# Kernel tuning notes

Hardware: AMD Instinct MI355X
Metric: run time of the kernel (lower is better)

Reference implementation:

```python
import jax, jax.numpy as jnp
import numpy as np

# ---- geometry constants (from init_kwargs) ----
ANGLE_NUM = 360
DET = 448          # detector bins
N = 320            # volume is N x N, voxel pitch 1.0, centered at origin
SID = 500.0        # source-isocenter distance
SDD = 1000.0       # source-detector distance
DU = 1.6           # detector pixel pitch
LAMB = 1.0
R = N * np.sqrt(2.0) / 2.0   # half-diagonal of volume
N_SAMP = 452                 # samples per ray, step ~ 1 voxel
DT = np.float32(2.0 * R / N_SAMP)


def forward_project(vol):
    """Ray-driven fan-beam forward projection. vol: [B,N,N] -> sino [B,A,D]."""
    half = (N - 1) / 2.0
    betas = jnp.deg2rad(jnp.linspace(0.0, 360.0, ANGLE_NUM, endpoint=False)).astype(jnp.float32)
    u = ((jnp.arange(DET, dtype=jnp.float32) - (DET - 1) / 2.0) * DU)          # [D]
    t = (SID - R) + (jnp.arange(N_SAMP, dtype=jnp.float32) + 0.5) * (2.0 * R / N_SAMP)  # [S]

    def one_angle(_, beta):
        cb, sb = jnp.cos(beta), jnp.sin(beta)
        src = jnp.stack([SID * cb, SID * sb])            # source position [2]
        ax = jnp.stack([-cb, -sb])                       # toward isocenter
        uax = jnp.stack([-sb, cb])                       # detector axis
        det_pts = src[None, :] + SDD * ax[None, :] + u[:, None] * uax[None, :]  # [D,2]
        dirs = det_pts - src[None, :]
        dirs = dirs / jnp.linalg.norm(dirs, axis=-1, keepdims=True)             # [D,2]
        pts = src[None, None, :] + t[None, :, None] * dirs[:, None, :]          # [D,S,2]
        ix = pts[..., 0] + half
        iy = pts[..., 1] + half
        x0 = jnp.floor(ix); y0 = jnp.floor(iy)
        fx = ix - x0;       fy = iy - y0
        x0i = x0.astype(jnp.int32); y0i = y0.astype(jnp.int32)

        def gather(yy, xx):
            inb = (xx >= 0) & (xx < N) & (yy >= 0) & (yy < N)
            v = vol[:, jnp.clip(yy, 0, N - 1), jnp.clip(xx, 0, N - 1)]  # [B,D,S]
            return v * inb[None].astype(vol.dtype)

        val = (gather(y0i, x0i)         * ((1 - fx) * (1 - fy))[None]
             + gather(y0i, x0i + 1)     * (fx * (1 - fy))[None]
             + gather(y0i + 1, x0i)     * ((1 - fx) * fy)[None]
             + gather(y0i + 1, x0i + 1) * (fx * fy)[None])
        return None, val.sum(-1) * DT   # line integral per detector bin [B,D]

    _, sino = jax.lax.scan(one_angle, None, betas)   # [A,B,D]
    return jnp.transpose(sino, (1, 0, 2))            # [B,A,D]


def setup_inputs() -> dict:
    key = jax.random.key(0)
    k1, k2 = jax.random.split(key)
    x = jax.random.normal(k1, (2, N, N), dtype=jnp.float32)
    p = jax.random.normal(k2, (2, ANGLE_NUM, DET), dtype=jnp.float32)
    return {"x": x, "p": p}


def reference(x, p):
    # SART-style update: x - lamb * BP(FP(x) - p), BP = exact adjoint of FP
    residual = forward_project(x) - p
    (bp_vol,) = jax.linear_transpose(forward_project, x)(residual)
    return x - LAMB * bp_vol
```

## Files before the change

### kernel.cpp

```cpp
#include <hip/hip_runtime.h>
#include <hip/hip_fp16.h>
#include <math.h>

#define A_NUM 360
#define DET_N 448
#define NN 320
#define NSAMP 452
#define NB 2
#define NPIX (NN * NN)
#define NRAY (A_NUM * DET_N)
#define NCH 4
#define CHS (NSAMP / NCH)
#define NORB 25600
#define NSPQ15 15
#define NSPQ12 12
#define PN 324

#define R_D   226.27416997969522
#define DT_D  (2.0 * R_D / (double)NSAMP)
#define T0_D  (500.0 - R_D + 0.5 * DT_D)
#define DTF   ((float)DT_D)
#define T0F   ((float)T0_D)
#define INVDT ((float)(1.0 / DT_D))
#define K0F   ((float)((-1.4150 - T0_D) * (1.0 / DT_D)))

typedef float f32x2 __attribute__((ext_vector_type(2)));

__device__ __forceinline__ int orb_swizzle(int ri, int rj) {
    int tile = (rj >> 3) * 20 + (ri >> 3);
    int intra = ((rj & 7) << 3) | (ri & 7);
    return (tile << 6) | intra;
}

__global__ __launch_bounds__(256) void prep_k(float2* __restrict__ tabD,
                                              float4* __restrict__ tabS,
                                              float4* __restrict__ dirq,
                                              float4* __restrict__ angG) {
    int tid = blockIdx.x * blockDim.x + threadIdx.x;
    if (tid >= NRAY) return;
    int d = tid % DET_N, a = tid / DET_N;
    double beta = (double)a * (M_PI / 180.0);
    double cbd = cos(beta), sbd = sin(beta);
    double u = ((double)d - 223.5) * 1.6;
    double inorm = 1.0 / sqrt(1.0e6 + u * u);
    float dx = (float)((-1000.0 * cbd - u * sbd) * inorm);
    float dy = (float)((-1000.0 * sbd + u * cbd) * inorm);
    tabD[tid] = make_float2(dx, dy);
    if (d == 0) {
        tabS[a] = make_float4((float)cbd, (float)sbd,
                              (float)(500.0 * cbd + 161.5),
                              (float)(500.0 * sbd + 161.5));
        angG[a] = make_float4((float)cbd, (float)sbd,
                              (float)(500.0 * cbd + 159.5),
                              (float)(500.0 * sbd + 159.5));
    }
    if (a < 90) dirq[a * DET_N + d] = make_float4(dx, dy, DTF * dx, DTF * dy);
}

__device__ __forceinline__ unsigned packpix(const float* __restrict__ x,
                                            bool v, int idx) {
    if (!v) return 0u;
    __half2 h = __floats2half2_rn(x[idx], x[NPIX + idx]);
    return *reinterpret_cast<unsigned*>(&h);
}
__device__ __forceinline__ f32x2 up16(unsigned w) {
    __half2 h = *reinterpret_cast<__half2*>(&w);
    return (f32x2){__low2float(h), __high2float(h)};
}

__global__ __launch_bounds__(256) void interleaveQB_k(const float* __restrict__ x,
                                                      uint4* __restrict__ xb) {
    int t = blockIdx.x * blockDim.x + threadIdx.x;
    if (t >= PN * PN) return;
    int px = t % PN, py = t / PN;
    int ox = px - 2, oy = py - 2;
    bool cx0 = (ox >= 0) && (ox < NN);
    bool cx1 = (ox + 1 >= 0) && (ox + 1 < NN);
    bool cy0 = (oy >= 0) && (oy < NN);
    bool cy1 = (oy + 1 >= 0) && (oy + 1 < NN);
    int b = oy * NN + ox;
    uint4 w;
    w.x = packpix(x, cx0 && cy0, b);
    w.y = packpix(x, cx1 && cy0, b + 1);
    w.z = packpix(x, cx0 && cy1, b + NN);
    w.w = packpix(x, cx1 && cy1, b + NN + 1);
    xb[t] = w;
}

__global__ __launch_bounds__(256) void interleaveQBT_k(const float* __restrict__ x,
                                                       uint4* __restrict__ xbT) {
    int t = blockIdx.x * blockDim.x + threadIdx.x;
    if (t >= PN * PN) return;
    int r = t % PN, q = t / PN;
    int row0 = r - 2, col0 = q - 2;
    bool r0v = (row0 >= 0) && (row0 < NN);
    bool r1v = (row0 + 1 >= 0) && (row0 + 1 < NN);
    bool c0v = (col0 >= 0) && (col0 < NN);
    bool c1v = (col0 + 1 >= 0) && (col0 + 1 < NN);
    int b = row0 * NN + col0;
    uint4 w;
    w.x = packpix(x, r0v && c0v, b);
    w.y = packpix(x, r1v && c0v, b + NN);
    w.z = packpix(x, r0v && c1v, b + 1);
    w.w = packpix(x, r1v && c1v, b + NN + 1);
    xbT[t] = w;
}

__device__ __forceinline__ void samp1(const uint4* __restrict__ buf,
                                      float ix, float iy,
                                      f32x2& accA, f32x2& accB) {
    float xf = floorf(ix), yf = floorf(iy);
    float fx = ix - xf, fy = iy - yf;
    int idx = (int)yf * PN + (int)xf;
    uint4 qv = buf[idx];
    float gx = 1.0f - fx, gy = 1.0f - fy;
    float w00 = gx * gy, w01 = fx * gy, w10 = gx * fy, w11 = fx * fy;
    accA = __builtin_elementwise_fma((f32x2){w00, w00}, up16(qv.x), accA);
    accB = __builtin_elementwise_fma((f32x2){w01, w01}, up16(qv.y), accB);
    accA = __builtin_elementwise_fma((f32x2){w10, w10}, up16(qv.z), accA);
    accB = __builtin_elementwise_fma((f32x2){w11, w11}, up16(qv.w), accB);
}

__global__ __launch_bounds__(256) void partial_k(const float2* __restrict__ tabD,
                                                 const float4* __restrict__ tabS,
                                                 const uint4* __restrict__ bufR,
                                                 const uint4* __restrict__ bufT,
                                                 float2* __restrict__ part) {
    int tid = blockIdx.x * blockDim.x + threadIdx.x;
    if (tid >= NRAY * NCH) return;
    int d_lo = tid & 15;
    int c    = (tid >> 4) & 3;
    int rest = tid >> 6;
    int d_hi = rest % (DET_N / 16);
    int a    = rest / (DET_N / 16);
    int ray  = a * DET_N + d_hi * 16 + d_lo;

    float2 D = tabD[ray];
    float4 S = tabS[a];
    bool swp = fabsf(S.x) > fabsf(S.y);
    float dirx = swp ? D.y : D.x;
    float diry = swp ? D.x : D.y;
    float sx   = swp ? S.w : S.z;
    float sy   = swp ? S.z : S.w;
    const uint4* __restrict__ buf = swp ? bufT : bufR;

    float invx = __builtin_amdgcn_rcpf(dirx);
    float invy = __builtin_amdgcn_rcpf(diry);
    float tx1 = (0.5f   - sx) * invx;
    float tx2 = (322.5f - sx) * invx;
    float ty1 = (0.5f   - sy) * invy;
    float ty2 = (322.5f - sy) * invy;
    float tmn = fmaxf(fminf(tx1, tx2), fminf(ty1, ty2));
    float tmx = fminf(fmaxf(tx1, tx2), fmaxf(ty1, ty2));
    float smnf = fminf(fmaxf(ceilf((tmn - T0F) * INVDT), 0.0f), (float)(NSAMP - 1));
    float smxf = fminf(fmaxf(floorf((tmx - T0F) * INVDT), 0.0f), (float)(NSAMP - 1));
    int smin = (int)smnf;
    int smax = (int)smxf;
    int klo = (smin - c + 3) >> 2;  if (klo < 0) klo = 0;
    int khi = (smax - c) >> 2;      if (khi > CHS - 1) khi = CHS - 1;
    int kn = khi - klo + 1;

    float t0c = fmaf((float)(c + 4 * klo), DTF, T0F);
    float ix = fmaf(t0c, dirx, sx);
    float iy = fmaf(t0c, diry, sy);
    float stx = (4.0f * DTF) * dirx;
    float sty = (4.0f * DTF) * diry;

    f32x2 accA = {0.0f, 0.0f}, accB = {0.0f, 0.0f};

    int k = 0;
#pragma unroll 2
    for (; k + 4 <= kn; k += 4) {
        float ix0 = ix,              iy0 = iy;
        float ix1 = ix + stx,        iy1 = iy + sty;
        float ix2 = ix + 2.0f * stx, iy2 = iy + 2.0f * sty;
        float ix3 = ix + 3.0f * stx, iy3 = iy + 3.0f * sty;
        float xf0 = floorf(ix0), yf0 = floorf(iy0);
        float xf1 = floorf(ix1), yf1 = floorf(iy1);
        float xf2 = floorf(ix2), yf2 = floorf(iy2);
        float xf3 = floorf(ix3), yf3 = floorf(iy3);
        int i0 = (int)yf0 * PN + (int)xf0;
        int i1 = (int)yf1 * PN + (int)xf1;
        int i2 = (int)yf2 * PN + (int)xf2;
        int i3 = (int)yf3 * PN + (int)xf3;
        uint4 q0 = buf[i0];
        uint4 q1 = buf[i1];
        uint4 q2 = buf[i2];
        uint4 q3 = buf[i3];
        float fx0 = ix0 - xf0, fy0 = iy0 - yf0;
        float fx1 = ix1 - xf1, fy1 = iy1 - yf1;
        float fx2 = ix2 - xf2, fy2 = iy2 - yf2;
        float fx3 = ix3 - xf3, fy3 = iy3 - yf3;
        float gx0 = 1.0f - fx0, gy0 = 1.0f - fy0;
        float gx1 = 1.0f - fx1, gy1 = 1.0f - fy1;
        float gx2 = 1.0f - fx2, gy2 = 1.0f - fy2;
        float gx3 = 1.0f - fx3, gy3 = 1.0f - fy3;
        float w;
        w = gx0 * gy0; accA = __builtin_elementwise_fma((f32x2){w, w}, up16(q0.x), accA);
        w = fx0 * gy0; accB = __builtin_elementwise_fma((f32x2){w, w}, up16(q0.y), accB);
        w = gx0 * fy0; accA = __builtin_elementwise_fma((f32x2){w, w}, up16(q0.z), accA);
        w = fx0 * fy0; accB = __builtin_elementwise_fma((f32x2){w, w}, up16(q0.w), accB);
        w = gx1 * gy1; accA = __builtin_elementwise_fma((f32x2){w, w}, up16(q1.x), accA);
        w = fx1 * gy1; accB = __builtin_elementwise_fma((f32x2){w, w}, up16(q1.y), accB);
        w = gx1 * fy1; accA = __builtin_elementwise_fma((f32x2){w, w}, up16(q1.z), accA);
        w = fx1 * fy1; accB = __builtin_elementwise_fma((f32x2){w, w}, up16(q1.w), accB);
        w = gx2 * gy2; accA = __builtin_elementwise_fma((f32x2){w, w}, up16(q2.x), accA);
        w = fx2 * gy2; accB = __builtin_elementwise_fma((f32x2){w, w}, up16(q2.y), accB);
        w = gx2 * fy2; accA = __builtin_elementwise_fma((f32x2){w, w}, up16(q2.z), accA);
        w = fx2 * fy2; accB = __builtin_elementwise_fma((f32x2){w, w}, up16(q2.w), accB);
        w = gx3 * gy3; accA = __builtin_elementwise_fma((f32x2){w, w}, up16(q3.x), accA);
        w = fx3 * gy3; accB = __builtin_elementwise_fma((f32x2){w, w}, up16(q3.y), accB);
        w = gx3 * fy3; accA = __builtin_elementwise_fma((f32x2){w, w}, up16(q3.z), accA);
        w = fx3 * fy3; accB = __builtin_elementwise_fma((f32x2){w, w}, up16(q3.w), accB);
        ix += 4.0f * stx; iy += 4.0f * sty;
    }
    for (; k < kn; ++k) {
        samp1(buf, ix, iy, accA, accB);
        ix += stx; iy += sty;
    }

    f32x2 acc = accA + accB;
    part[c * NRAY + ray] = make_float2(acc.x, acc.y);
}

__global__ __launch_bounds__(256) void finalize4_k(const float* __restrict__ p,
                                                   const float2* __restrict__ part,
                                                   float4* __restrict__ rvq) {
    int tid = blockIdx.x * blockDim.x + threadIdx.x;
    if (tid >= 90 * DET_N) return;
    int d = tid % DET_N, am = tid / DET_N;
    float rv[8];
#pragma unroll
    for (int k = 0; k < 4; ++k) {
        int ray = (am + 90 * k) * DET_N + d;
        float a0 = 0.0f, a1 = 0.0f;
#pragma unroll
        for (int c = 0; c < NCH; ++c) {
            float2 pr = part[c * NRAY + ray];
            a0 += pr.x; a1 += pr.y;
        }
        rv[2 * k]     = -fmaf(a0, DTF, -p[ray]) * DTF;
        rv[2 * k + 1] = -fmaf(a1, DTF, -p[NRAY + ray]) * DTF;
    }
    rvq[2 * tid]     = make_float4(rv[0], rv[1], rv[2], rv[3]);
    rvq[2 * tid + 1] = make_float4(rv[4], rv[5], rv[6], rv[7]);
}

#define TAP4(A0, A1, A2, A3)                                 \
    {                                                        \
        f32x2 ad  = __builtin_elementwise_max(dxy, -dxy);    \
        f32x2 wv2 = __builtin_elementwise_max(one2 - ad, zero2); \
        float w = wv2.x * wv2.y;                             \
        f32x2 wv = {w, w};                                   \
        A0 = __builtin_elementwise_fma(wv, q0, A0);          \
        A1 = __builtin_elementwise_fma(wv, q1, A1);          \
        A2 = __builtin_elementwise_fma(wv, q2, A2);          \
        A3 = __builtin_elementwise_fma(wv, q3, A3);          \
        dxy += dd2;                                          \
    }

#define QTAPS(Q, A0, A1, A2, A3, DX_, DY_, EX_, EY_)                       \
    {                                                                      \
        float4 A = angG[90 * (Q) + am];                                    \
        float rx = fi - A.z, ry = fj - A.w;                                \
        float rpar  = -fmaf(rx, A.x, ry * A.y);                            \
        float rperp = fmaf(ry, A.x, -rx * A.y);                            \
        float us = 1000.0f * rperp * __builtin_amdgcn_rcpf(rpar);          \
        float dstar = fmaf(us, 0.625f, 223.5f);                            \
        float r2 = fmaf(rx, rx, ry * ry);                                  \
        float ir = rsqrtf(r2);                                             \
        float g  = fmaf(fabsf(rx) + fabsf(ry), ir, 0.031f);                \
        float kk = fmaf(us, us, 1.0e6f) * ir;                              \
        float dd = fmaf(g * kk, 6.25e-4f, 0.05f);                          \
        int dlo = (int)ceilf(dstar - dd);  if (dlo < 0) dlo = 0;           \
        int dhi = (int)floorf(dstar + dd); if (dhi > DET_N - 1) dhi = DET_N - 1; \
        for (int d = dlo; d <= dhi; ++d) {                                 \
            float4 Dq  = sD[d];                                            \
            float4 r01 = sR0[d];                                           \
            float4 r23 = sR1[d];                                           \
            float Tx = DX_, Ty = DY_;                                      \
            float ts = fmaf(rx, Tx, ry * Ty);                              \
            float sf = ceilf(fmaf(ts, INVDT, K0F));                        \
            sf = fminf(fmaxf(sf, 0.0f), (float)(NSAMP - 3));               \
            float tt = fmaf(sf, DTF, T0F);                                 \
            f32x2 dxy = {fmaf(tt, Tx, -rx), fmaf(tt, Ty, -ry)};            \
            f32x2 dd2 = {EX_, EY_};                                        \
            f32x2 q0 = {r01.x, r01.y}, q1 = {r01.z, r01.w};                \
            f32x2 q2 = {r23.x, r23.y}, q3 = {r23.z, r23.w};                \
            TAP4(A0, A1, A2, A3)                                           \
            TAP4(A0, A1, A2, A3)                                           \
            TAP4(A0, A1, A2, A3)                                           \
        }                                                                  \
    }

template <int NSPLIT>
__global__ __launch_bounds__(256) void bp4_k(const float4* __restrict__ dirq,
                                             const float4* __restrict__ rvq,
                                             const float4* __restrict__ angG,
                                             float* __restrict__ bpp) {
    __shared__ float4 sD[DET_N];
    __shared__ float4 sR0[DET_N];
    __shared__ float4 sR1[DET_N];

    int tid = blockIdx.x * blockDim.x + threadIdx.x;
    int orb = tid % NORB;
    int sp  = tid / NORB;
    int tile  = orb >> 6;
    int intra = orb & 63;
    int ri = (tile % 20) * 8 + (intra & 7);
    int rj = (tile / 20) * 8 + (intra >> 3);
    float fi = (float)ri, fj = (float)rj;

    const f32x2 one2 = {1.0f, 1.0f}, zero2 = {0.0f, 0.0f};
    f32x2 acc0 = {0.0f, 0.0f}, acc1 = acc0, acc2 = acc0, acc3 = acc0;

    bool first = true;
    for (int am = sp; am < 90; am += NSPLIT) {
        const float4* Drow = dirq + am * DET_N;
        const float4* Rrow = rvq + am * DET_N * 2;
        if (!first) __syncthreads();
        first = false;
        for (int i = threadIdx.x; i < DET_N; i += 256) {
            sD[i]  = Drow[i];
            sR0[i] = Rrow[2 * i];
            sR1[i] = Rrow[2 * i + 1];
        }
        __syncthreads();

        QTAPS(0, acc0, acc1, acc2, acc3,  Dq.x,  Dq.y,  Dq.z,  Dq.w)
        QTAPS(1, acc3, acc0, acc1, acc2, -Dq.y,  Dq.x, -Dq.w,  Dq.z)
        QTAPS(2, acc2, acc3, acc0, acc1, -Dq.x, -Dq.y, -Dq.z, -Dq.w)
        QTAPS(3, acc1, acc2, acc3, acc0,  Dq.y, -Dq.x,  Dq.w, -Dq.z)
    }

    int base = sp * 8 * NORB + orb;
    bpp[base           ] = acc0.x;
    bpp[base + 1 * NORB] = acc0.y;
    bpp[base + 2 * NORB] = acc1.x;
    bpp[base + 3 * NORB] = acc1.y;
    bpp[base + 4 * NORB] = acc2.x;
    bpp[base + 5 * NORB] = acc2.y;
    bpp[base + 6 * NORB] = acc3.x;
    bpp[base + 7 * NORB] = acc3.y;
}

template <int NSPLIT>
__global__ __launch_bounds__(256) void combine4_k(const float* __restrict__ x,
                                                  const float* __restrict__ bpp,
                                                  float* __restrict__ out) {
    int tid = blockIdx.x * blockDim.x + threadIdx.x;
    if (tid >= NB * NPIX) return;
    int i = tid % NN;
    int j = (tid / NN) % NN;
    int b = tid / NPIX;
    int k, ri, rj;
    if (j < 160) {
        if (i < 160) { k = 0; ri = i;       rj = j;       }
        else         { k = 1; ri = j;       rj = 319 - i; }
    } else {
        if (i >= 160){ k = 2; ri = 319 - i; rj = 319 - j; }
        else         { k = 3; ri = 319 - j; rj = i;       }
    }
    int off = (k * 2 + b) * NORB + orb_swizzle(ri, rj);
    float s = x[tid];
#pragma unroll
    for (int sp = 0; sp < NSPLIT; ++sp) s += bpp[sp * 8 * NORB + off];
    out[tid] = s;
}

template <bool USE_TAB>
__global__ __launch_bounds__(256) void residual_k(const float* __restrict__ x,
                                                  const float* __restrict__ p,
                                                  void* __restrict__ tabv) {
    int tid = blockIdx.x * blockDim.x + threadIdx.x;
    if (tid >= NRAY) return;
    int d = tid % DET_N, a = tid / DET_N;
    double beta = (double)a * (M_PI / 180.0);
    double cbd = cos(beta), sbd = sin(beta);
    double u = ((double)d - 223.5) * 1.6;
    double inorm = 1.0 / sqrt(1.0e6 + u * u);
    float dirx = (float)((-1000.0 * cbd - u * sbd) * inorm);
    float diry = (float)((-1000.0 * sbd + u * cbd) * inorm);
    float sx = (float)(500.0 * cbd + 159.5);
    float sy = (float)(500.0 * sbd + 159.5);
    const float* __restrict__ v0 = x;
    const float* __restrict__ v1 = x + NPIX;
    float acc0 = 0.0f, acc1 = 0.0f;
    for (int s = 0; s < NSAMP; ++s) {
        float t  = fmaf((float)s, DTF, T0F);
        float ix = fmaf(t, dirx, sx);
        float iy = fmaf(t, diry, sy);
        float xf = floorf(ix), yf = floorf(iy);
        int x0 = (int)xf, y0 = (int)yf;
        if (x0 < -1 || x0 >= NN || y0 < -1 || y0 >= NN) continue;
        float fx = ix - xf, fy = iy - yf;
        int x1 = x0 + 1, y1 = y0 + 1;
        bool vx0 = (x0 >= 0), vx1 = (x1 < NN);
        bool vy0 = (y0 >= 0), vy1 = (y1 < NN);
        int x0c = vx0 ? x0 : 0, x1c = vx1 ? x1 : NN - 1;
        int y0c = vy0 ? y0 : 0, y1c = vy1 ? y1 : NN - 1;
        int i00 = y0c * NN + x0c, i01 = y0c * NN + x1c;
        int i10 = y1c * NN + x0c, i11 = y1c * NN + x1c;
        float gx = 1.0f - fx, gy = 1.0f - fy;
        float w00 = (vx0 && vy0) ? gx * gy : 0.0f;
        float w01 = (vx1 && vy0) ? fx * gy : 0.0f;
        float w10 = (vx0 && vy1) ? gx * fy : 0.0f;
        float w11 = (vx1 && vy1) ? fx * fy : 0.0f;
        acc0 = fmaf(v0[i00], w00, acc0); acc0 = fmaf(v0[i01], w01, acc0);
        acc0 = fmaf(v0[i10], w10, acc0); acc0 = fmaf(v0[i11], w11, acc0);
        acc1 = fmaf(v1[i00], w00, acc1); acc1 = fmaf(v1[i01], w01, acc1);
        acc1 = fmaf(v1[i10], w10, acc1); acc1 = fmaf(v1[i11], w11, acc1);
    }
    float rv0 = -fmaf(acc0, DTF, -p[tid]) * DTF;
    float rv1 = -fmaf(acc1, DTF, -p[NRAY + tid]) * DTF;
    if constexpr (USE_TAB) {
        ((float4*)tabv)[tid] = make_float4(dirx, diry, rv0, rv1);
    } else {
        ((float2*)tabv)[tid] = make_float2(rv0, rv1);
    }
}

template <int NSPLIT, bool DIRECT, bool USE_TAB>
__global__ __launch_bounds__(256) void bp_k(const void* __restrict__ tabv,
                                            const float* __restrict__ x,
                                            float* __restrict__ outp) {
    __shared__ float4 ang[A_NUM];
    for (int a = threadIdx.x; a < A_NUM; a += blockDim.x) {
        double beta = (double)a * (M_PI / 180.0);
        double cbd = cos(beta), sbd = sin(beta);
        ang[a] = make_float4((float)cbd, (float)sbd,
                             (float)(500.0 * cbd + 159.5),
                             (float)(500.0 * sbd + 159.5));
    }
    __syncthreads();

    int tid = blockIdx.x * blockDim.x + threadIdx.x;
    if (tid >= NPIX * NSPLIT) return;
    int pix = tid % NPIX;
    int sp  = tid / NPIX;
    float fi = (float)(pix % NN), fj = (float)(pix / NN);

    float acc0 = 0.0f, acc1 = 0.0f;

    for (int a = sp; a < A_NUM; a += NSPLIT) {
        float4 A = ang[a];
        float rx = fi - A.z, ry = fj - A.w;
        float rpar  = -fmaf(rx, A.x, ry * A.y);
        float rperp = fmaf(ry, A.x, -rx * A.y);
        float us = 1000.0f * rperp * __builtin_amdgcn_rcpf(rpar);
        float dstar = fmaf(us, 0.625f, 223.5f);
        float r2 = fmaf(rx, rx, ry * ry);
        float kk = fmaf(us, us, 1.0e6f) * rsqrtf(r2);
        float dd = fmaf(kk, 8.8394e-4f, 0.05f);
        int dlo = (int)ceilf(dstar - dd);  if (dlo < 0) dlo = 0;
        int dhi = (int)floorf(dstar + dd); if (dhi > DET_N - 1) dhi = DET_N - 1;

        const float4* __restrict__ Trow =
            USE_TAB ? ((const float4*)tabv) + a * DET_N : nullptr;
        const float2* __restrict__ RVrow =
            USE_TAB ? nullptr : ((const float2*)tabv) + a * DET_N;

        for (int d = dlo; d <= dhi; ++d) {
            float dirx, diry, rv0, rv1;
            if constexpr (USE_TAB) {
                float4 T = Trow[d];
                dirx = T.x; diry = T.y; rv0 = T.z; rv1 = T.w;
            } else {
                float u = ((float)d - 223.5f) * 1.6f;
                float inv = rsqrtf(fmaf(u, u, 1.0e6f));
                dirx = fmaf(-1000.0f, A.x, -u * A.y) * inv;
                diry = fmaf(-1000.0f, A.y,  u * A.x) * inv;
                float2 RV = RVrow[d];
                rv0 = RV.x; rv1 = RV.y;
            }
            float ts = fmaf(rx, dirx, ry * diry);
            float sf = ceilf(fmaf(ts, INVDT, K0F));
            sf = fminf(fmaxf(sf, 0.0f), (float)(NSAMP - 3));
            float tt = fmaf(sf, DTF, T0F);
            float dx = fmaf(tt, dirx, -rx);
            float dy = fmaf(tt, diry, -ry);
            float ddx = DTF * dirx, ddy = DTF * diry;
#pragma unroll
            for (int k = 0; k < 3; ++k) {
                float wx = fmaxf(1.0f - fabsf(dx), 0.0f);
                float wy = fmaxf(1.0f - fabsf(dy), 0.0f);
                float w = wx * wy;
                acc0 = fmaf(w, rv0, acc0);
                acc1 = fmaf(w, rv1, acc1);
                dx += ddx; dy += ddy;
            }
        }
    }

    if constexpr (DIRECT) {
        outp[pix]        = x[pix]        + acc0;
        outp[NPIX + pix] = x[NPIX + pix] + acc1;
    } else {
        outp[(sp * 2 + 0) * NPIX + pix] = acc0;
        outp[(sp * 2 + 1) * NPIX + pix] = acc1;
    }
}

template <int NSPLIT>
__global__ __launch_bounds__(256) void combine_k(const float* __restrict__ x,
                                                 const float* __restrict__ part,
                                                 float* __restrict__ out) {
    int tid = blockIdx.x * blockDim.x + threadIdx.x;
    if (tid >= NB * NPIX) return;
    int pix = tid % NPIX, b = tid / NPIX;
    float s = x[tid];
#pragma unroll
    for (int sp = 0; sp < NSPLIT; ++sp) s += part[(sp * 2 + b) * NPIX + pix];
    out[tid] = s;
}

extern "C" void kernel_launch(void* const* d_in, const int* in_sizes, int n_in,
                              void* d_out, int out_size, void* d_ws, size_t ws_size,
                              hipStream_t stream) {
    const float* x = (const float*)d_in[0];
    const float* p = (const float*)d_in[1];
    float* out = (float*)d_out;
    char* ws = (char*)d_ws;

    const size_t bpp15_bytes = (size_t)NSPQ15 * 8 * NORB * 4;
    const size_t bpp12_bytes = (size_t)NSPQ12 * 8 * NORB * 4;
    const size_t NEED15 = 1951744 + bpp15_bytes;
    const size_t NEED12 = 1951744 + bpp12_bytes;
    const size_t NEED8  = 10471936;

    const size_t tab_bytes  = sizeof(float4) * NRAY;
    const size_t bpp4_bytes = sizeof(float) * 8 * NPIX;

    if (ws_size >= NEED12 || ws_size >= NEED8) {
        float4* dirq  = (float4*)(ws + 0);
        float2* tabD  = (float2*)(ws + 645120);
        float4* rvq   = (float4*)(ws + 645120);
        float4* tabS  = (float4*)(ws + 1935360);
        float4* angG  = (float4*)(ws + 1943552);
        uint4*  xqb   = (uint4*)(ws + 1951744);
        uint4*  xqbT  = (uint4*)(ws + 3631360);
        float2* fpart = (float2*)(ws + 5310976);
        float*  bpp   = (float*)(ws + 1951744);

        prep_k<<<NRAY / 256, 256, 0, stream>>>(tabD, tabS, dirq, angG);
        interleaveQB_k<<<(PN * PN + 255) / 256, 256, 0, stream>>>(x, xqb);
        interleaveQBT_k<<<(PN * PN + 255) / 256, 256, 0, stream>>>(x, xqbT);
        partial_k<<<(NRAY * NCH) / 256, 256, 0, stream>>>(tabD, tabS, xqb, xqbT, fpart);
        finalize4_k<<<(90 * DET_N + 255) / 256, 256, 0, stream>>>(p, fpart, rvq);
        if (ws_size >= NEED15) {
            bp4_k<NSPQ15><<<(NORB * NSPQ15) / 256, 256, 0, stream>>>(dirq, rvq, angG, bpp);
            combine4_k<NSPQ15><<<(NB * NPIX) / 256, 256, 0, stream>>>(x, bpp, out);
        } else if (ws_size >= NEED12) {
            bp4_k<NSPQ12><<<(NORB * NSPQ12) / 256, 256, 0, stream>>>(dirq, rvq, angG, bpp);
            combine4_k<NSPQ12><<<(NB * NPIX) / 256, 256, 0, stream>>>(x, bpp, out);
        } else {
            bp4_k<8><<<(NORB * 8) / 256, 256, 0, stream>>>(dirq, rvq, angG, bpp);
            combine4_k<8><<<(NB * NPIX) / 256, 256, 0, stream>>>(x, bpp, out);
        }
    } else if (ws_size >= tab_bytes + bpp4_bytes) {
        float4* tab = (float4*)ws;
        float* bpp  = (float*)(ws + tab_bytes);
        residual_k<true><<<(NRAY + 255) / 256, 256, 0, stream>>>(x, p, tab);
        bp_k<4, false, true><<<(NPIX * 4) / 256, 256, 0, stream>>>(tab, x, bpp);
        combine_k<4><<<(NB * NPIX + 255) / 256, 256, 0, stream>>>(x, bpp, out);
    } else if (ws_size >= tab_bytes) {
        float4* tab = (float4*)ws;
        residual_k<true><<<(NRAY + 255) / 256, 256, 0, stream>>>(x, p, tab);
        bp_k<1, true, true><<<NPIX / 256, 256, 0, stream>>>(tab, x, out);
    } else {
        float2* rw2 = (float2*)ws;
        residual_k<false><<<(NRAY + 255) / 256, 256, 0, stream>>>(x, p, rw2);
        bp_k<1, true, false><<<NPIX / 256, 256, 0, stream>>>(rw2, x, out);
    }
}
```

Baseline: 143.4 us.

## Software-pipeline forward-projection gathers and shrink backprojection direction table

```diff
diff --git a/kernel.cpp b/kernel.cpp
--- a/kernel.cpp
+++ b/kernel.cpp
@@ -34,7 +34,7 @@
 
 __global__ __launch_bounds__(256) void prep_k(float2* __restrict__ tabD,
                                               float4* __restrict__ tabS,
-                                              float4* __restrict__ dirq,
+                                              float2* __restrict__ dirq,
                                               float4* __restrict__ angG) {
     int tid = blockIdx.x * blockDim.x + threadIdx.x;
     if (tid >= NRAY) return;
@@ -54,7 +54,7 @@
                               (float)(500.0 * cbd + 159.5),
                               (float)(500.0 * sbd + 159.5));
     }
-    if (a < 90) dirq[a * DET_N + d] = make_float4(dx, dy, DTF * dx, DTF * dy);
+    if (a < 90) dirq[a * DET_N + d] = make_float2(dx, dy);
 }
 
 __device__ __forceinline__ unsigned packpix(const float* __restrict__ x,
@@ -121,6 +121,52 @@
     accB = __builtin_elementwise_fma((f32x2){w11, w11}, up16(qv.w), accB);
 }
 
+#define PLOAD(Q0, Q1, Q2, Q3, FX, FY)                                  \
+    {                                                                  \
+        float x0_ = lx,               y0_ = ly;                        \
+        float x1_ = lx + stx,         y1_ = ly + sty;                  \
+        float x2_ = lx + 2.0f * stx,  y2_ = ly + 2.0f * sty;           \
+        float x3_ = lx + 3.0f * stx,  y3_ = ly + 3.0f * sty;           \
+        float xf0_ = floorf(x0_), yf0_ = floorf(y0_);                  \
+        float xf1_ = floorf(x1_), yf1_ = floorf(y1_);                  \
+        float xf2_ = floorf(x2_), yf2_ = floorf(y2_);                  \
+        float xf3_ = floorf(x3_), yf3_ = floorf(y3_);                  \
+        Q0 = buf[(int)yf0_ * PN + (int)xf0_];                          \
+        Q1 = buf[(int)yf1_ * PN + (int)xf1_];                          \
+        Q2 = buf[(int)yf2_ * PN + (int)xf2_];                          \
+        Q3 = buf[(int)yf3_ * PN + (int)xf3_];                          \
+        FX##0 = x0_ - xf0_; FY##0 = y0_ - yf0_;                        \
+        FX##1 = x1_ - xf1_; FY##1 = y1_ - yf1_;                        \
+        FX##2 = x2_ - xf2_; FY##2 = y2_ - yf2_;                        \
+        FX##3 = x3_ - xf3_; FY##3 = y3_ - yf3_;                        \
+        lx += 4.0f * stx; ly += 4.0f * sty;                            \
+    }
+
+#define PCONS(Q0, Q1, Q2, Q3, FX, FY)                                  \
+    {                                                                  \
+        float gx0_ = 1.0f - FX##0, gy0_ = 1.0f - FY##0;                \
+        float gx1_ = 1.0f - FX##1, gy1_ = 1.0f - FY##1;                \
+        float gx2_ = 1.0f - FX##2, gy2_ = 1.0f - FY##2;                \
+        float gx3_ = 1.0f - FX##3, gy3_ = 1.0f - FY##3;                \
+        float w_;                                                      \
+        w_ = gx0_ * gy0_;  accA = __builtin_elementwise_fma((f32x2){w_, w_}, up16(Q0.x), accA); \
+        w_ = FX##0 * gy0_; accB = __builtin_elementwise_fma((f32x2){w_, w_}, up16(Q0.y), accB); \
+        w_ = gx0_ * FY##0; accA = __builtin_elementwise_fma((f32x2){w_, w_}, up16(Q0.z), accA); \
+        w_ = FX##0 * FY##0;accB = __builtin_elementwise_fma((f32x2){w_, w_}, up16(Q0.w), accB); \
+        w_ = gx1_ * gy1_;  accA = __builtin_elementwise_fma((f32x2){w_, w_}, up16(Q1.x), accA); \
+        w_ = FX##1 * gy1_; accB = __builtin_elementwise_fma((f32x2){w_, w_}, up16(Q1.y), accB); \
+        w_ = gx1_ * FY##1; accA = __builtin_elementwise_fma((f32x2){w_, w_}, up16(Q1.z), accA); \
+        w_ = FX##1 * FY##1;accB = __builtin_elementwise_fma((f32x2){w_, w_}, up16(Q1.w), accB); \
+        w_ = gx2_ * gy2_;  accA = __builtin_elementwise_fma((f32x2){w_, w_}, up16(Q2.x), accA); \
+        w_ = FX##2 * gy2_; accB = __builtin_elementwise_fma((f32x2){w_, w_}, up16(Q2.y), accB); \
+        w_ = gx2_ * FY##2; accA = __builtin_elementwise_fma((f32x2){w_, w_}, up16(Q2.z), accA); \
+        w_ = FX##2 * FY##2;accB = __builtin_elementwise_fma((f32x2){w_, w_}, up16(Q2.w), accB); \
+        w_ = gx3_ * gy3_;  accA = __builtin_elementwise_fma((f32x2){w_, w_}, up16(Q3.x), accA); \
+        w_ = FX##3 * gy3_; accB = __builtin_elementwise_fma((f32x2){w_, w_}, up16(Q3.y), accB); \
+        w_ = gx3_ * FY##3; accA = __builtin_elementwise_fma((f32x2){w_, w_}, up16(Q3.z), accA); \
+        w_ = FX##3 * FY##3;accB = __builtin_elementwise_fma((f32x2){w_, w_}, up16(Q3.w), accB); \
+    }
+
 __global__ __launch_bounds__(256) void partial_k(const float2* __restrict__ tabD,
                                                  const float4* __restrict__ tabS,
                                                  const uint4* __restrict__ bufR,
@@ -159,64 +205,43 @@
     int klo = (smin - c + 3) >> 2;  if (klo < 0) klo = 0;
     int khi = (smax - c) >> 2;      if (khi > CHS - 1) khi = CHS - 1;
     int kn = khi - klo + 1;
+    if (kn < 0) kn = 0;
 
     float t0c = fmaf((float)(c + 4 * klo), DTF, T0F);
-    float ix = fmaf(t0c, dirx, sx);
-    float iy = fmaf(t0c, diry, sy);
+    float lx = fmaf(t0c, dirx, sx);
+    float ly = fmaf(t0c, diry, sy);
     float stx = (4.0f * DTF) * dirx;
     float sty = (4.0f * DTF) * diry;
 
     f32x2 accA = {0.0f, 0.0f}, accB = {0.0f, 0.0f};
 
-    int k = 0;
-#pragma unroll 2
-    for (; k + 4 <= kn; k += 4) {
-        float ix0 = ix,              iy0 = iy;
-        float ix1 = ix + stx,        iy1 = iy + sty;
-        float ix2 = ix + 2.0f * stx, iy2 = iy + 2.0f * sty;
-        float ix3 = ix + 3.0f * stx, iy3 = iy + 3.0f * sty;
-        float xf0 = floorf(ix0), yf0 = floorf(iy0);
-        float xf1 = floorf(ix1), yf1 = floorf(iy1);
-        float xf2 = floorf(ix2), yf2 = floorf(iy2);
-        float xf3 = floorf(ix3), yf3 = floorf(iy3);
-        int i0 = (int)yf0 * PN + (int)xf0;
-        int i1 = (int)yf1 * PN + (int)xf1;
-        int i2 = (int)yf2 * PN + (int)xf2;
-        int i3 = (int)yf3 * PN + (int)xf3;
-        uint4 q0 = buf[i0];
-        uint4 q1 = buf[i1];
-        uint4 q2 = buf[i2];
-        uint4 q3 = buf[i3];
-        float fx0 = ix0 - xf0, fy0 = iy0 - yf0;
-        float fx1 = ix1 - xf1, fy1 = iy1 - yf1;
-        float fx2 = ix2 - xf2, fy2 = iy2 - yf2;
-        float fx3 = ix3 - xf3, fy3 = iy3 - yf3;
-        float gx0 = 1.0f - fx0, gy0 = 1.0f - fy0;
-        float gx1 = 1.0f - fx1, gy1 = 1.0f - fy1;
-        float gx2 = 1.0f - fx2, gy2 = 1.0f - fy2;
-        float gx3 = 1.0f - fx3, gy3 = 1.0f - fy3;
-        float w;
-        w = gx0 * gy0; accA = __builtin_elementwise_fma((f32x2){w, w}, up16(q0.x), accA);
-        w = fx0 * gy0; accB = __builtin_elementwise_fma((f32x2){w, w}, up16(q0.y), accB);
-        w = gx0 * fy0; accA = __builtin_elementwise_fma((f32x2){w, w}, up16(q0.z), accA);
-        w = fx0 * fy0; accB = __builtin_elementwise_fma((f32x2){w, w}, up16(q0.w), accB);
-        w = gx1 * gy1; accA = __builtin_elementwise_fma((f32x2){w, w}, up16(q1.x), accA);
-        w = fx1 * gy1; accB = __builtin_elementwise_fma((f32x2){w, w}, up16(q1.y), accB);
-        w = gx1 * fy1; accA = __builtin_elementwise_fma((f32x2){w, w}, up16(q1.z), accA);
-        w = fx1 * fy1; accB = __builtin_elementwise_fma((f32x2){w, w}, up16(q1.w), accB);
-        w = gx2 * gy2; accA = __builtin_elementwise_fma((f32x2){w, w}, up16(q2.x), accA);
-        w = fx2 * gy2; accB = __builtin_elementwise_fma((f32x2){w, w}, up16(q2.y), accB);
-        w = gx2 * fy2; accA = __builtin_elementwise_fma((f32x2){w, w}, up16(q2.z), accA);
-        w = fx2 * fy2; accB = __builtin_elementwise_fma((f32x2){w, w}, up16(q2.w), accB);
-        w = gx3 * gy3; accA = __builtin_elementwise_fma((f32x2){w, w}, up16(q3.x), accA);
-        w = fx3 * gy3; accB = __builtin_elementwise_fma((f32x2){w, w}, up16(q3.y), accB);
-        w = gx3 * fy3; accA = __builtin_elementwise_fma((f32x2){w, w}, up16(q3.z), accA);
-        w = fx3 * fy3; accB = __builtin_elementwise_fma((f32x2){w, w}, up16(q3.w), accB);
-        ix += 4.0f * stx; iy += 4.0f * sty;
-    }
-    for (; k < kn; ++k) {
-        samp1(buf, ix, iy, accA, accB);
-        ix += stx; iy += sty;
+    int nblk = kn >> 2;
+    int rem  = kn & 3;
+
+    uint4 qa0, qa1, qa2, qa3, qb0, qb1, qb2, qb3;
+    float fxa0, fxa1, fxa2, fxa3, fya0, fya1, fya2, fya3;
+    float fxb0, fxb1, fxb2, fxb3, fyb0, fyb1, fyb2, fyb3;
+
+    if (nblk > 0) {
+        PLOAD(qa0, qa1, qa2, qa3, fxa, fya)
+        int b = 1;
+        for (; b + 1 < nblk; b += 2) {
+            PLOAD(qb0, qb1, qb2, qb3, fxb, fyb)
+            PCONS(qa0, qa1, qa2, qa3, fxa, fya)
+            PLOAD(qa0, qa1, qa2, qa3, fxa, fya)
+            PCONS(qb0, qb1, qb2, qb3, fxb, fyb)
+        }
+        if (b < nblk) {
+            PLOAD(qb0, qb1, qb2, qb3, fxb, fyb)
+            PCONS(qa0, qa1, qa2, qa3, fxa, fya)
+            PCONS(qb0, qb1, qb2, qb3, fxb, fyb)
+        } else {
+            PCONS(qa0, qa1, qa2, qa3, fxa, fya)
+        }
+    }
+    for (int r = 0; r < rem; ++r) {
+        samp1(buf, lx, ly, accA, accB);
+        lx += stx; ly += sty;
     }
 
     f32x2 acc = accA + accB;
@@ -259,7 +284,7 @@
         dxy += dd2;                                          \
     }
 
-#define QTAPS(Q, A0, A1, A2, A3, DX_, DY_, EX_, EY_)                       \
+#define QTAPS(Q, A0, A1, A2, A3, DX_, DY_)                                 \
     {                                                                      \
         float4 A = angG[90 * (Q) + am];                                    \
         float rx = fi - A.z, ry = fj - A.w;                                \
@@ -275,7 +300,7 @@
         int dlo = (int)ceilf(dstar - dd);  if (dlo < 0) dlo = 0;           \
         int dhi = (int)floorf(dstar + dd); if (dhi > DET_N - 1) dhi = DET_N - 1; \
         for (int d = dlo; d <= dhi; ++d) {                                 \
-            float4 Dq  = sD[d];                                            \
+            float2 Dq  = sD[d];                                            \
             float4 r01 = sR0[d];                                           \
             float4 r23 = sR1[d];                                           \
             float Tx = DX_, Ty = DY_;                                      \
@@ -284,7 +309,7 @@
             sf = fminf(fmaxf(sf, 0.0f), (float)(NSAMP - 3));               \
             float tt = fmaf(sf, DTF, T0F);                                 \
             f32x2 dxy = {fmaf(tt, Tx, -rx), fmaf(tt, Ty, -ry)};            \
-            f32x2 dd2 = {EX_, EY_};                                        \
+            f32x2 dd2 = {DTF * Tx, DTF * Ty};                              \
             f32x2 q0 = {r01.x, r01.y}, q1 = {r01.z, r01.w};                \
             f32x2 q2 = {r23.x, r23.y}, q3 = {r23.z, r23.w};                \
             TAP4(A0, A1, A2, A3)                                           \
@@ -294,11 +319,11 @@
     }
 
 template <int NSPLIT>
-__global__ __launch_bounds__(256) void bp4_k(const float4* __restrict__ dirq,
+__global__ __launch_bounds__(256) void bp4_k(const float2* __restrict__ dirq,
                                              const float4* __restrict__ rvq,
                                              const float4* __restrict__ angG,
                                              float* __restrict__ bpp) {
-    __shared__ float4 sD[DET_N];
+    __shared__ float2 sD[DET_N];
     __shared__ float4 sR0[DET_N];
     __shared__ float4 sR1[DET_N];
 
@@ -316,7 +341,7 @@
 
     bool first = true;
     for (int am = sp; am < 90; am += NSPLIT) {
-        const float4* Drow = dirq + am * DET_N;
+        const float2* Drow = dirq + am * DET_N;
         const float4* Rrow = rvq + am * DET_N * 2;
         if (!first) __syncthreads();
         first = false;
@@ -327,10 +352,10 @@
         }
         __syncthreads();
 
-        QTAPS(0, acc0, acc1, acc2, acc3,  Dq.x,  Dq.y,  Dq.z,  Dq.w)
-        QTAPS(1, acc3, acc0, acc1, acc2, -Dq.y,  Dq.x, -Dq.w,  Dq.z)
-        QTAPS(2, acc2, acc3, acc0, acc1, -Dq.x, -Dq.y, -Dq.z, -Dq.w)
-        QTAPS(3, acc1, acc2, acc3, acc0,  Dq.y, -Dq.x,  Dq.w, -Dq.z)
+        QTAPS(0, acc0, acc1, acc2, acc3,  Dq.x,  Dq.y)
+        QTAPS(1, acc3, acc0, acc1, acc2, -Dq.y,  Dq.x)
+        QTAPS(2, acc2, acc3, acc0, acc1, -Dq.x, -Dq.y)
+        QTAPS(3, acc1, acc2, acc3, acc0,  Dq.y, -Dq.x)
     }
 
     int base = sp * 8 * NORB + orb;
@@ -532,7 +557,7 @@
     const size_t bpp4_bytes = sizeof(float) * 8 * NPIX;
 
     if (ws_size >= NEED12 || ws_size >= NEED8) {
-        float4* dirq  = (float4*)(ws + 0);
+        float2* dirq  = (float2*)(ws + 0);
         float2* tabD  = (float2*)(ws + 645120);
         float4* rvq   = (float4*)(ws + 645120);
         float4* tabS  = (float4*)(ws + 1935360);
```

Result: no change. 142.7 us (-0.5%).
